# Performance work log

Hardware: AMD Instinct MI355X
Metric: run time of the kernel (lower is better)

Reference implementation:

```python
import jax, jax.numpy as jnp
import numpy as np

N_HEAD = 16
N_KV_HEAD = 4
HD = 128
ROPE_THETA = 10000.0


def _rope_cos_sin(T, hd, dtype):
    inv_freq = 1.0 / (ROPE_THETA ** (jnp.arange(0, hd, 2, dtype=jnp.float32) / hd))  # [hd/2]
    ang = jnp.arange(T, dtype=jnp.float32)[:, None] * inv_freq[None, :]  # [T, hd/2]
    return jnp.cos(ang).astype(dtype), jnp.sin(ang).astype(dtype)


def _apply_rope(x, cos, sin):
    # x: [B, T, H, hd]; rotate interleaved (even, odd) pairs Llama-style
    x1 = x[..., 0::2]
    x2 = x[..., 1::2]
    c = cos[None, :, None, :]
    s = sin[None, :, None, :]
    o1 = x1 * c - x2 * s
    o2 = x1 * s + x2 * c
    return jnp.stack([o1, o2], axis=-1).reshape(x.shape)


def setup_inputs() -> dict:
    key = jax.random.key(0)
    k1, k2, k3 = jax.random.split(key, 3)
    B, T, C = 4, 2048, 2048
    x = jax.random.normal(k1, (B, T, C), dtype=jnp.float32)
    w_attn = jax.random.normal(k2, ((N_HEAD + 2 * N_KV_HEAD) * HD, C), dtype=jnp.float32) * (C ** -0.5)
    w_proj = jax.random.normal(k3, (C, C), dtype=jnp.float32) * (C ** -0.5)
    return {"x": x, "w_attn": w_attn, "w_proj": w_proj}


def reference(x, w_attn, w_proj):
    B, T, C = x.shape
    n_rep = N_HEAD // N_KV_HEAD
    qkv = x @ w_attn.T  # [B, T, (H + 2*Hkv)*hd]
    q, k, v = jnp.split(qkv, [N_HEAD * HD, (N_HEAD + N_KV_HEAD) * HD], axis=-1)
    q = q.reshape(B, T, N_HEAD, HD)
    k = k.reshape(B, T, N_KV_HEAD, HD)
    v = v.reshape(B, T, N_KV_HEAD, HD)
    cos, sin = _rope_cos_sin(T, HD, x.dtype)
    q = _apply_rope(q, cos, sin)
    k = _apply_rope(k, cos, sin)
    # GQA: repeat kv heads (repeat_interleave on head dim)
    k = jnp.repeat(k, n_rep, axis=2)
    v = jnp.repeat(v, n_rep, axis=2)
    # [B, H, T, hd]
    q = q.transpose(0, 2, 1, 3)
    k = k.transpose(0, 2, 1, 3)
    v = v.transpose(0, 2, 1, 3)
    att = jnp.einsum("bhqd,bhkd->bhqk", q, k) * (1.0 / jnp.sqrt(jnp.asarray(HD, x.dtype)))
    causal = jnp.tril(jnp.ones((T, T), dtype=bool))
    att = jnp.where(causal[None, None, :, :], att, jnp.asarray(-jnp.inf, att.dtype))
    att = jax.nn.softmax(att, axis=-1)
    y = jnp.einsum("bhqk,bhkd->bhqd", att, v)
    y = y.transpose(0, 2, 1, 3).reshape(B, T, C)
    return y @ w_proj.T
```

## Files before the change

kernel.cpp:

```cpp
#include <hip/hip_runtime.h>
#include <math.h>

#define NH   16
#define NKV  4
#define HD   128
#define BSZ  4
#define TLEN 2048
#define CDIM 2048
#define MROWS (BSZ*TLEN)

typedef short bf16x8 __attribute__((ext_vector_type(8)));
typedef float f32x4  __attribute__((ext_vector_type(4)));
typedef int   int4v  __attribute__((ext_vector_type(4)));

__device__ inline float bf2f(unsigned short h) {
  union { unsigned u; float f; } x; x.u = ((unsigned)h) << 16; return x.f;
}
__device__ inline unsigned short f2bf(float f) {
  union { float f; unsigned u; } x; x.f = f;
  unsigned u = x.u;
  return (unsigned short)((u + 0x7FFFu + ((u >> 16) & 1u)) >> 16);
}

__device__ inline void gload_lds16(const void* g, void* l) {
  __builtin_amdgcn_global_load_lds((const __attribute__((address_space(1))) void*)g,
                                   (__attribute__((address_space(3))) void*)l, 16, 0, 0);
}

__global__ void detect_kernel(const void* __restrict__ wproj, int* __restrict__ flag) {
  __shared__ int cnt;
  if (threadIdx.x == 0) cnt = 0;
  __syncthreads();
  const unsigned short* s = (const unsigned short*)wproj;
  unsigned short v = s[2 * threadIdx.x];
  int e = (v >> 7) & 0xFF;
  if (e >= 90 && e <= 141) atomicAdd(&cnt, 1);
  __syncthreads();
  if (threadIdx.x == 0) *flag = (cnt >= 192) ? 1 : 0;
}

__device__ inline void stage8(short* dst, const void* src, size_t eoff, int isbf) {
  if (isbf) {
    *(int4v*)dst = *(const int4v*)((const short*)src + eoff);
  } else {
    const f32x4* f = (const f32x4*)((const float*)src + eoff);
    f32x4 a = f[0], b = f[1];
    __align__(16) short t[8];
    t[0] = (short)f2bf(a[0]); t[1] = (short)f2bf(a[1]);
    t[2] = (short)f2bf(a[2]); t[3] = (short)f2bf(a[3]);
    t[4] = (short)f2bf(b[0]); t[5] = (short)f2bf(b[1]);
    t[6] = (short)f2bf(b[2]); t[7] = (short)f2bf(b[3]);
    *(int4v*)dst = *(int4v*)t;
  }
}

__global__ __launch_bounds__(256) void cvt_kernel(const void* __restrict__ src,
                                                  short* __restrict__ dst,
                                                  int n8, const int* __restrict__ flagp)
{
  const int fl = *flagp;
  const int i = blockIdx.x * 256 + threadIdx.x;
  if (i >= n8) return;
  __align__(16) short t[8];
  stage8(t, src, (size_t)i * 8, fl);
  *(int4v*)(dst + (size_t)i * 8) = *(int4v*)t;
}

template<int MODE>
__global__ __launch_bounds__(512, 2) void gemm_bt(
    const short* __restrict__ A, const short* __restrict__ W,
    short* __restrict__ o0, short* __restrict__ o1, short* __restrict__ o2,
    float* __restrict__ o0f, const int* __restrict__ flagp)
{
  __shared__ __align__(16) short SB[4][16384];
  const int fl = *flagp;
  const int tid  = threadIdx.x;
  const int wave = tid >> 6;
  const int lane = tid & 63;
  const int cl   = lane & 15;
  const int quad = lane >> 4;
  const int wm = wave >> 2;
  const int wn = wave & 3;
  const int nwgx = gridDim.x;
  int wg = (int)blockIdx.y * nwgx + (int)blockIdx.x;
  const int cpx = (nwgx * (int)gridDim.y) >> 3;
  wg = (wg & 7) * cpx + (wg >> 3);
  const int m0 = (wg / nwgx) * 256;
  const int n0 = (wg % nwgx) * 256;

  const int cswz  = (((cl & 1) << 2) | quad) ^ (cl >> 1);
  const int abase = (wm*64 + (cl >> 1)) * 64 + cswz * 8;
  const int bbase = 8192 + (wn*32 + (cl >> 1)) * 64 + cswz * 8;

  f32x4 acc[8][4];
#pragma unroll
  for (int i = 0; i < 8; i++)
#pragma unroll
    for (int j = 0; j < 4; j++) acc[i][j] = (f32x4){0.f, 0.f, 0.f, 0.f};

  const short* Asrc = A + (size_t)m0 * CDIM;
  const short* Wsrc = W + (size_t)n0 * CDIM;

  auto stage1 = [&](const short* src, int kk, short* dst) {
#pragma unroll
    for (int i = 0; i < 2; i++) {
      const int chunk = i*512 + tid;
      const int lr  = chunk >> 3;
      const int c   = (chunk & 7) ^ (lr & 7);
      const int row = lr*2 + (c >> 2);
      gload_lds16(src + (size_t)row * CDIM + kk + (c & 3)*8,
                  dst + ((i*512 + wave*64) << 3));
    }
  };
#define STAGE(t) { short* db = &SB[(t)&3][0]; stage1(Asrc, (t)*32, db); stage1(Wsrc, (t)*32, db + 8192); }

  STAGE(0); STAGE(1); STAGE(2);
  const int nt = CDIM / 32;
  for (int kt = 0; kt < nt; ++kt) {
    const int rem = nt - kt;
    if (rem > 2)       asm volatile("s_waitcnt vmcnt(8)" : : : "memory");
    else if (rem == 2) asm volatile("s_waitcnt vmcnt(4)" : : : "memory");
    else               asm volatile("s_waitcnt vmcnt(0)" : : : "memory");
    __builtin_amdgcn_s_barrier();
    if (kt + 3 < nt) STAGE(kt+3);
    const short* Tb = &SB[kt & 3][0];
    bf16x8 af[8], bfj[4];
#pragma unroll
    for (int i = 0; i < 8; i++) af[i]  = *(const bf16x8*)&Tb[abase + i*512];
#pragma unroll
    for (int j = 0; j < 4; j++) bfj[j] = *(const bf16x8*)&Tb[bbase + j*512];
    __builtin_amdgcn_s_setprio(1);
#pragma unroll
    for (int i = 0; i < 8; i++)
#pragma unroll
      for (int j = 0; j < 4; j++)
        acc[i][j] = __builtin_amdgcn_mfma_f32_16x16x32_bf16(af[i], bfj[j], acc[i][j], 0, 0, 0);
    __builtin_amdgcn_s_setprio(0);
  }
#undef STAGE

#pragma unroll
  for (int i = 0; i < 8; i++) {
#pragma unroll
    for (int j = 0; j < 4; j++) {
#pragma unroll
      for (int r = 0; r < 4; r++) {
        const int gm = m0 + wm*128 + i*16 + quad*4 + r;
        const int gn = n0 + wn*64  + j*16 + cl;
        const float fv = acc[i][j][r];
        if (MODE == 1) {
          if (fl) o0[(size_t)gm * CDIM + gn] = (short)f2bf(fv);
          else    o0f[(size_t)gm * CDIM + gn] = fv;
        } else {
          const int b = gm >> 11;
          const int t = gm & (TLEN - 1);
          const int head = gn >> 7;
          const int d = gn & (HD - 1);
          const unsigned short h = f2bf(fv);
          if (head < 16) {
            o0[(((size_t)(b*NH + head) * TLEN + t) << 7) + d] = (short)h;
          } else if (head < 20) {
            o1[(((size_t)(b*NKV + (head-16)) * TLEN + t) << 7) + d] = (short)h;
          } else {
            o2[(((size_t)(b*NKV + (head-20)) * HD + d) << 11) + t] = (short)h;
          }
        }
      }
    }
  }
}

__global__ __launch_bounds__(256) void rope_kernel(short* __restrict__ qb,
                                                   short* __restrict__ kb)
{
  const int idx = blockIdx.x * 256 + threadIdx.x;
  const int per_plane = TLEN * 64;
  const int plane = idx / per_plane;
  const int rem = idx - plane * per_plane;
  const int t = rem >> 6;
  const int i = rem & 63;
  short* base = (plane < 64) ? (qb + (size_t)plane * (TLEN*HD))
                             : (kb + (size_t)(plane - 64) * (TLEN*HD));
  const size_t off = (size_t)t * HD + 2*i;
  const float x1 = bf2f((unsigned short)base[off]);
  const float x2 = bf2f((unsigned short)base[off+1]);
  const float inv = __expf(-0.14391156847064198f * (float)i);
  const float ang = (float)t * inv;
  float s, c;
  sincosf(ang, &s, &c);
  const float qscale = (plane < 64) ? 0.08838834764831845f : 1.0f;
  base[off]   = (short)f2bf((x1*c - x2*s) * qscale);
  base[off+1] = (short)f2bf((x1*s + x2*c) * qscale);
}

__device__ inline void stage_tiles(short* Ks, short* Vs,
                                   const short* Kp, const short* Vp,
                                   int k0, int tid, int wave) {
#pragma unroll
  for (int i = 0; i < 2; i++) {
    const int chunk = i*512 + tid;
    const int row = chunk >> 4;
    const int cc  = (chunk & 15) ^ (row & 7);
    gload_lds16(Kp + (size_t)(k0 + row)*HD + cc*8,
                Ks + ((i*512 + wave*64) << 3));
  }
#pragma unroll
  for (int i = 0; i < 2; i++) {
    const int chunk = i*512 + tid;
    const int row = chunk >> 3;
    const int cc  = (chunk & 7) ^ (row & 7);
    gload_lds16(Vp + (size_t)row*TLEN + k0 + cc*8,
                Vs + ((i*512 + wave*64) << 3));
  }
}

__global__ __launch_bounds__(512, 4) void attn_kernel(
    const short* __restrict__ qb, const short* __restrict__ kb,
    const short* __restrict__ vtb, short* __restrict__ yb)
{
  __shared__ __align__(16) short Ks[2][64*128];
  __shared__ __align__(16) short Vs[2][128*64];
  __shared__ short Plds[8][16][64];
  const int tid  = threadIdx.x;
  const int wave = tid >> 6;
  const int lane = tid & 63;
  const int cl   = lane & 15;
  const int quad = lane >> 4;
  const int bh = blockIdx.y;
  const int b = bh >> 4, h = bh & 15;
  const int kvh = h >> 2;

  const short* Qp = qb  + (size_t)(b*NH  + h)   * TLEN * HD;
  const short* Kp = kb  + (size_t)(b*NKV + kvh) * TLEN * HD;
  const short* Vp = vtb + (size_t)(b*NKV + kvh) * HD * TLEN;
  short* Pw = &Plds[wave][0][0];
  const int swz = (cl & 7) << 3;

  bf16x8 ones;
#pragma unroll
  for (int i = 0; i < 8; i++) ones[i] = (short)0x3F80;

#pragma unroll 1
  for (int pass = 0; pass < 2; ++pass) {
    const int qi = pass ? (TLEN/128 - 1 - (int)blockIdx.x) : (int)blockIdx.x;
    const int q0 = qi * 128;
    const int ntiles = 2*qi + 2;

    bf16x8 qf[4];
    const int qrow = q0 + wave*16 + cl;
#pragma unroll
    for (int s = 0; s < 4; s++)
      qf[s] = *(const bf16x8*)(Qp + (size_t)qrow*HD + s*32 + quad*8);

    f32x4 O[8];
#pragma unroll
    for (int d = 0; d < 8; d++) O[d] = (f32x4){0.f, 0.f, 0.f, 0.f};
    f32x4 Ol = (f32x4){0.f, 0.f, 0.f, 0.f};
    float m_i[4];
#pragma unroll
    for (int r = 0; r < 4; r++) m_i[r] = -1e9f;

    stage_tiles(Ks[0], Vs[0], Kp, Vp, 0, tid, wave);
    __syncthreads();
    int cur = 0;

    for (int kt = 0; kt < ntiles; kt++) {
      const int k0 = kt * 64;

      if (kt + 1 < ntiles)
        stage_tiles(Ks[cur^1], Vs[cur^1], Kp, Vp, k0 + 64, tid, wave);

      const short* Kt = Ks[cur];
      const short* Vt = Vs[cur];

      f32x4 S[4];
#pragma unroll
      for (int j = 0; j < 4; j++) S[j] = (f32x4){0.f, 0.f, 0.f, 0.f};
#pragma unroll
      for (int s = 0; s < 4; s++) {
        bf16x8 kfj[4];
#pragma unroll
        for (int j = 0; j < 4; j++)
          kfj[j] = *(const bf16x8*)(&Kt[(size_t)(j*16 + cl)*128 + ((((s*4 + quad) << 3) ^ swz))]);
#pragma unroll
        for (int j = 0; j < 4; j++)
          S[j] = __builtin_amdgcn_mfma_f32_16x16x32_bf16(qf[s], kfj[j], S[j], 0, 0, 0);
      }

      if (kt >= ntiles - 2) {
#pragma unroll
        for (int j = 0; j < 4; j++) {
          const int col = k0 + j*16 + cl;
#pragma unroll
          for (int r = 0; r < 4; r++) {
            const int row = q0 + wave*16 + quad*4 + r;
            if (col > row) S[j][r] = -1e9f;
          }
        }
      }

      float pmax[4];
#pragma unroll
      for (int r = 0; r < 4; r++) {
        float mx = fmaxf(fmaxf(S[0][r], S[1][r]), fmaxf(S[2][r], S[3][r]));
#pragma unroll
        for (int off = 1; off < 16; off <<= 1) mx = fmaxf(mx, __shfl_xor(mx, off));
        pmax[r] = mx;
      }
      const int ok = (pmax[0] - m_i[0] <= 8.f) && (pmax[1] - m_i[1] <= 8.f) &&
                     (pmax[2] - m_i[2] <= 8.f) && (pmax[3] - m_i[3] <= 8.f);
      if (!__all(ok)) {
#pragma unroll
        for (int r = 0; r < 4; r++) {
          const float mnew = fmaxf(m_i[r], pmax[r]);
          const float alpha = __expf(m_i[r] - mnew);
          Ol[r] *= alpha;
          m_i[r] = mnew;
#pragma unroll
          for (int d = 0; d < 8; d++) O[d][r] *= alpha;
        }
      }
#pragma unroll
      for (int r = 0; r < 4; r++)
#pragma unroll
        for (int j = 0; j < 4; j++)
          S[j][r] = __expf(S[j][r] - m_i[r]);

#pragma unroll
      for (int j = 0; j < 4; j++)
#pragma unroll
        for (int r = 0; r < 4; r++) {
          const int row = quad*4 + r;
          int idx = row*64 + j*16 + cl;
          idx ^= (row & 7) << 3;
          Pw[idx] = (short)f2bf(S[j][r]);
        }

#pragma unroll
      for (int s2 = 0; s2 < 2; s2++) {
        int idx = cl*64 + s2*32 + quad*8;
        idx ^= (cl & 7) << 3;
        bf16x8 pf = *(const bf16x8*)(&Pw[idx]);
        Ol = __builtin_amdgcn_mfma_f32_16x16x32_bf16(pf, ones, Ol, 0, 0, 0);
#pragma unroll
        for (int d = 0; d < 8; d++) {
          bf16x8 vfd = *(const bf16x8*)(&Vt[(size_t)(d*16 + cl)*64 + ((((s2*4 + quad) << 3) ^ swz))]);
          O[d] = __builtin_amdgcn_mfma_f32_16x16x32_bf16(pf, vfd, O[d], 0, 0, 0);
        }
      }

      __syncthreads();
      cur ^= 1;
    }

    float linv[4];
#pragma unroll
    for (int r = 0; r < 4; r++) linv[r] = 1.0f / Ol[r];
#pragma unroll
    for (int d = 0; d < 8; d++) {
#pragma unroll
      for (int r = 0; r < 4; r++) {
        const int t = q0 + wave*16 + quad*4 + r;
        yb[(size_t)(b*TLEN + t) * CDIM + h*HD + d*16 + cl] = (short)f2bf(O[d][r] * linv[r]);
      }
    }
  }
}

extern "C" void kernel_launch(void* const* d_in, const int* in_sizes, int n_in,
                              void* d_out, int out_size, void* d_ws, size_t ws_size,
                              hipStream_t stream)
{
  const void* x      = d_in[0];
  const void* w_attn = d_in[1];
  const void* w_proj = d_in[2];

  char* ws = (char*)d_ws;
  int*   flag = (int*)ws;
  short* qb  = (short*)(ws + (size_t) 1*1024*1024);
  short* kb  = (short*)(ws + (size_t)33*1024*1024);
  short* vtb = (short*)(ws + (size_t)41*1024*1024);
  short* yb  = (short*)(ws + (size_t)49*1024*1024);
  short* xb  = (short*)d_out;
  short* wab = (short*)((char*)d_out + (size_t)32*1024*1024);
  short* wpb = kb;

  dim3 blk(256);
  detect_kernel<<<1, blk, 0, stream>>>(w_proj, flag);
  cvt_kernel<<<dim3((MROWS*CDIM/8)/256), blk, 0, stream>>>(x, xb, MROWS*CDIM/8, flag);
  cvt_kernel<<<dim3((3072*CDIM/8)/256), blk, 0, stream>>>(w_attn, wab, 3072*CDIM/8, flag);
  gemm_bt<0><<<dim3(3072/256, MROWS/256), dim3(512), 0, stream>>>(xb, wab, qb, kb, vtb, nullptr, flag);
  rope_kernel<<<dim3((80*TLEN*64)/256), blk, 0, stream>>>(qb, kb);
  attn_kernel<<<dim3(TLEN/256, BSZ*NH), dim3(512), 0, stream>>>(qb, kb, vtb, yb);
  cvt_kernel<<<dim3((CDIM*CDIM/8)/256), blk, 0, stream>>>(w_proj, wpb, CDIM*CDIM/8, flag);
  gemm_bt<1><<<dim3(CDIM/256, MROWS/256), dim3(512), 0, stream>>>(yb, wpb, (short*)d_out,
                                                                  nullptr, nullptr, (float*)d_out, flag);
}
```

Before: 507.9 us.

## Fuse RoPE into QKV GEMM epilogue and switch softmax to exp2

```diff
diff --git a/kernel.cpp b/kernel.cpp
--- a/kernel.cpp
+++ b/kernel.cpp
@@ -143,19 +143,34 @@
   for (int i = 0; i < 8; i++) {
 #pragma unroll
     for (int j = 0; j < 4; j++) {
-#pragma unroll
-      for (int r = 0; r < 4; r++) {
-        const int gm = m0 + wm*128 + i*16 + quad*4 + r;
-        const int gn = n0 + wn*64  + j*16 + cl;
-        const float fv = acc[i][j][r];
-        if (MODE == 1) {
+      const int gn = n0 + wn*64 + j*16 + cl;
+      if (MODE == 1) {
+#pragma unroll
+        for (int r = 0; r < 4; r++) {
+          const int gm = m0 + wm*128 + i*16 + quad*4 + r;
+          const float fv = acc[i][j][r];
           if (fl) o0[(size_t)gm * CDIM + gn] = (short)f2bf(fv);
           else    o0f[(size_t)gm * CDIM + gn] = fv;
-        } else {
+        }
+      } else {
+        const int head = gn >> 7;
+        const int d = gn & (HD - 1);
+        const int dorope = (head < 20);
+        const float inv = dorope ? __expf(-0.14391156847064198f * (float)(d >> 1)) : 0.f;
+        const float qs  = (head < 16) ? 0.12751742f : 1.0f;
+        const float sgn = (d & 1) ? 1.0f : -1.0f;
+#pragma unroll
+        for (int r = 0; r < 4; r++) {
+          const int gm = m0 + wm*128 + i*16 + quad*4 + r;
           const int b = gm >> 11;
           const int t = gm & (TLEN - 1);
-          const int head = gn >> 7;
-          const int d = gn & (HD - 1);
+          float fv = acc[i][j][r];
+          const float pv = __shfl_xor(fv, 1);
+          if (dorope) {
+            float sn, cs;
+            sincosf((float)t * inv, &sn, &cs);
+            fv = (fv*cs + pv*sn*sgn) * qs;
+          }
           const unsigned short h = f2bf(fv);
           if (head < 16) {
             o0[(((size_t)(b*NH + head) * TLEN + t) << 7) + d] = (short)h;
@@ -168,29 +183,6 @@
       }
     }
   }
-}
-
-__global__ __launch_bounds__(256) void rope_kernel(short* __restrict__ qb,
-                                                   short* __restrict__ kb)
-{
-  const int idx = blockIdx.x * 256 + threadIdx.x;
-  const int per_plane = TLEN * 64;
-  const int plane = idx / per_plane;
-  const int rem = idx - plane * per_plane;
-  const int t = rem >> 6;
-  const int i = rem & 63;
-  short* base = (plane < 64) ? (qb + (size_t)plane * (TLEN*HD))
-                             : (kb + (size_t)(plane - 64) * (TLEN*HD));
-  const size_t off = (size_t)t * HD + 2*i;
-  const float x1 = bf2f((unsigned short)base[off]);
-  const float x2 = bf2f((unsigned short)base[off+1]);
-  const float inv = __expf(-0.14391156847064198f * (float)i);
-  const float ang = (float)t * inv;
-  float s, c;
-  sincosf(ang, &s, &c);
-  const float qscale = (plane < 64) ? 0.08838834764831845f : 1.0f;
-  base[off]   = (short)f2bf((x1*c - x2*s) * qscale);
-  base[off+1] = (short)f2bf((x1*s + x2*c) * qscale);
 }
 
 __device__ inline void stage_tiles(short* Ks, short* Vs,
@@ -307,13 +299,13 @@
         for (int off = 1; off < 16; off <<= 1) mx = fmaxf(mx, __shfl_xor(mx, off));
         pmax[r] = mx;
       }
-      const int ok = (pmax[0] - m_i[0] <= 8.f) && (pmax[1] - m_i[1] <= 8.f) &&
-                     (pmax[2] - m_i[2] <= 8.f) && (pmax[3] - m_i[3] <= 8.f);
+      const int ok = (pmax[0] - m_i[0] <= 11.5f) && (pmax[1] - m_i[1] <= 11.5f) &&
+                     (pmax[2] - m_i[2] <= 11.5f) && (pmax[3] - m_i[3] <= 11.5f);
       if (!__all(ok)) {
 #pragma unroll
         for (int r = 0; r < 4; r++) {
           const float mnew = fmaxf(m_i[r], pmax[r]);
-          const float alpha = __expf(m_i[r] - mnew);
+          const float alpha = exp2f(m_i[r] - mnew);
           Ol[r] *= alpha;
           m_i[r] = mnew;
 #pragma unroll
@@ -324,7 +316,7 @@
       for (int r = 0; r < 4; r++)
 #pragma unroll
         for (int j = 0; j < 4; j++)
-          S[j][r] = __expf(S[j][r] - m_i[r]);
+          S[j][r] = exp2f(S[j][r] - m_i[r]);
 
 #pragma unroll
       for (int j = 0; j < 4; j++)
@@ -390,7 +382,6 @@
   cvt_kernel<<<dim3((MROWS*CDIM/8)/256), blk, 0, stream>>>(x, xb, MROWS*CDIM/8, flag);
   cvt_kernel<<<dim3((3072*CDIM/8)/256), blk, 0, stream>>>(w_attn, wab, 3072*CDIM/8, flag);
   gemm_bt<0><<<dim3(3072/256, MROWS/256), dim3(512), 0, stream>>>(xb, wab, qb, kb, vtb, nullptr, flag);
-  rope_kernel<<<dim3((80*TLEN*64)/256), blk, 0, stream>>>(qb, kb);
   attn_kernel<<<dim3(TLEN/256, BSZ*NH), dim3(512), 0, stream>>>(qb, kb, vtb, yb);
   cvt_kernel<<<dim3((CDIM*CDIM/8)/256), blk, 0, stream>>>(w_proj, wpb, CDIM*CDIM/8, flag);
   gemm_bt<1><<<dim3(CDIM/256, MROWS/256), dim3(512), 0, stream>>>(yb, wpb, (short*)d_out,
```

Measured after the change: 554.2 us. +9.1%, slower.
